# Optimization experiments

Measured on AMD Instinct MI355X. Metric: run time of the kernel, lower is better.

## Reference

```python
import jax, jax.numpy as jnp
import numpy as np

B, T, H, V = 512, 256, 512, 7  # batch, decode steps, hidden_size, output_size (LSTM input fixed at 7)


def setup_inputs() -> dict:
    key = jax.random.key(0)
    ks = jax.random.split(key, 9)
    s = 1.0 / np.sqrt(H)  # pytorch LSTM/Linear default uniform init scale
    tgt_ids = jax.random.randint(ks[0], (B, T), 0, V)
    target_onehot = jax.nn.one_hot(tgt_ids, V, dtype=jnp.float32)
    return {
        "h0": jax.random.normal(ks[1], (B, H), jnp.float32),
        "c0": jax.random.normal(ks[2], (B, H), jnp.float32),
        "target_onehot": target_onehot,
        "W_ih": jax.random.uniform(ks[3], (4 * H, V), jnp.float32, -s, s),
        "W_hh": jax.random.uniform(ks[4], (4 * H, H), jnp.float32, -s, s),
        "b_ih": jax.random.uniform(ks[5], (4 * H,), jnp.float32, -s, s),
        "b_hh": jax.random.uniform(ks[6], (4 * H,), jnp.float32, -s, s),
        "W_out": jax.random.uniform(ks[7], (V, H), jnp.float32, -s, s),
        "b_out": jax.random.uniform(ks[8], (V,), jnp.float32, -s, s),
    }


def reference(h0, c0, target_onehot, W_ih, W_hh, b_ih, b_hh, W_out, b_out):
    # Faithful to DecoderRNN.forward with target_onehot given:
    #  - torch.rand(1)<0 is always False => teacher forcing never used
    #  - topi==5 early break only applies when target_onehot is None
    # => deterministic greedy decode: x0 = target_onehot[:,0], x_{t+1} = one_hot(argmax(logits_t))
    T_ = target_onehot.shape[1]
    bias = b_ih + b_hh

    def step(carry, _):
        h, c, x = carry  # h,c: [B,H]; x: [B,V]
        xr = jax.nn.relu(x)  # F.relu(input) in forward_step
        gates = xr @ W_ih.T + h @ W_hh.T + bias  # [B,4H], torch gate order i,f,g,o
        i_, f_, g_, o_ = jnp.split(gates, 4, axis=-1)
        c_new = jax.nn.sigmoid(f_) * c + jax.nn.sigmoid(i_) * jnp.tanh(g_)
        h_new = jax.nn.sigmoid(o_) * jnp.tanh(c_new)
        out = h_new @ W_out.T + b_out  # [B,V]
        nxt = jax.nn.one_hot(jnp.argmax(out, axis=-1), out.shape[-1], dtype=out.dtype)
        return (h_new, c_new, nxt), out

    (hT, cT, _), outs = jax.lax.scan(step, (h0, c0, target_onehot[:, 0]), None, length=T_)
    logp = jax.nn.log_softmax(jnp.transpose(outs, (1, 0, 2)), axis=-1)  # [B,T,V]
    return logp, hT, cT
```

## Files before the change

### kernel.cpp

```cpp
#include <hip/hip_runtime.h>
#include <hip/hip_bf16.h>
#include <math.h>

#define Bn 512
#define Tn 256
#define Hn 512
#define Vn 7
#define BH (Bn*Hn)
#define NLP (Bn*Tn*Vn)

#define NBLK 256
#define NTHR 512
#define NGRP 16
#define GBLK 16
#define CNT_STRIDE 32

#define RST 132
#define REDH (32*RST)


typedef short short8 __attribute__((ext_vector_type(8)));
typedef float f32x4  __attribute__((ext_vector_type(4)));

__device__ __forceinline__ float sigf(float x){ return 1.0f/(1.0f + expf(-x)); }

__device__ __forceinline__ void bsplit(float x, short &h, short &m, short &l){
    __hip_bfloat16 bh = __float2bfloat16(x);
    float fh = __bfloat162float(bh);
    float r1 = x - fh;
    __hip_bfloat16 bm = __float2bfloat16(r1);
    float fm = __bfloat162float(bm);
    float r2 = r1 - fm;
    __hip_bfloat16 bl = __float2bfloat16(r2);
    h = __builtin_bit_cast(short, bh);
    m = __builtin_bit_cast(short, bm);
    l = __builtin_bit_cast(short, bl);
}

struct Trip { short8 h, m, l; };

__device__ __forceinline__ Trip split8(const float4 &a, const float4 &b){
    Trip t;
    const float v[8] = {a.x, a.y, a.z, a.w, b.x, b.y, b.z, b.w};
    #pragma unroll
    for (int e = 0; e < 8; ++e){
        short hh, mm, ll;
        bsplit(v[e], hh, mm, ll);
        t.h[e] = hh; t.m[e] = mm; t.l[e] = ll;
    }
    return t;
}

__device__ __forceinline__ void group_barrier(int* cnt, int target){
    __syncthreads();
    if (threadIdx.x == 0){
        __hip_atomic_fetch_add(cnt, 1, __ATOMIC_RELEASE, __HIP_MEMORY_SCOPE_AGENT);
        while (__hip_atomic_load(cnt, __ATOMIC_RELAXED, __HIP_MEMORY_SCOPE_AGENT) < target)
            __builtin_amdgcn_s_sleep(1);
        (void)__hip_atomic_load(cnt, __ATOMIC_ACQUIRE, __HIP_MEMORY_SCOPE_AGENT);
    }
    __syncthreads();
}

__global__ void init_kernel(float* lp, int* cnts){
    int i = blockIdx.x*blockDim.x + threadIdx.x;
    if (i < NGRP) cnts[i*CNT_STRIDE] = 0;
    for (int x = i; x < NLP; x += (int)(gridDim.x*blockDim.x)) lp[x] = 0.0f;
}

__global__ void __launch_bounds__(NTHR, 2)
decoder_rnn_kernel(const float* __restrict__ h0, const float* __restrict__ c0,
                   const float* __restrict__ tgt, const float* __restrict__ Wih,
                   const float* __restrict__ Whh, const float* __restrict__ bih,
                   const float* __restrict__ bhh, const float* __restrict__ Wout,
                   const float* __restrict__ bout, float* out, float* ws)
{
    __shared__ float red[2*32*RST];
    __shared__ float hn_lds[32*33];
    __shared__ int   idx_lds[32];

    float* hbuf = ws;
    float* cws  = ws + 2*BH;
    int*   cnts = (int*)(ws + 3*BH);
    float* lp   = out;

    const int idx = blockIdx.x;
    const int jt  = ((idx & 7) << 1) | ((idx >> 7) & 1);
    const int bt  = (idx >> 3) & 15;
    const int b0  = bt << 5;
    const int j0  = jt << 5;

    const int tid  = threadIdx.x;
    const int wv   = tid >> 6;
    const int lane = tid & 63;
    const int kh   = wv & 1;
    const int gp   = wv >> 1;
    const int lr   = lane & 15;
    const int lk   = lane >> 4;
    int* cnt = cnts + bt*CNT_STRIDE;

    const int lg_bl = tid / 7, lg_v = tid % 7;

    long aoff0, aoff1, woff0, woff1;
    {
        const int kb = (kh << 8) + (lk << 3);
        aoff0 = (long)(b0 + lr)*Hn + kb;
        aoff1 = aoff0 + (long)16*Hn;
        woff0 = (long)((gp << 9) + j0 + lr)*Hn + kb;
        woff1 = woff0 + (long)16*Hn;
    }

    #pragma unroll
    for (int i = 0; i < 8; ++i){
        const int f = tid + (i << 9);
        const int r = f >> 7, c4 = f & 127;
        *(float4*)(hbuf + (long)(b0 + r)*Hn + (c4 << 2)) =
            *(const float4*)(h0 + (long)(b0 + r)*Hn + (c4 << 2));
    }
    if (tid < 256){
        const int r = tid >> 3, c4 = tid & 7;
        *(float4*)(cws + (long)(b0 + r)*Hn + j0 + (c4 << 2)) =
            *(const float4*)(c0 + (long)(b0 + r)*Hn + j0 + (c4 << 2));
    }
    __syncthreads();

    for (int t = 0; t < Tn; ++t){
        const float* hprev = hbuf + (t & 1)*BH;
        float*       hnext = hbuf + ((t + 1) & 1)*BH;

        if (tid < 32){
            const int  bl = tid;
            const long b  = b0 + bl;
            float best; int am = 0;
            if (t == 0){
                const float* xp = tgt + (b*Tn)*Vn;
                best = xp[0];
                #pragma unroll
                for (int v = 1; v < Vn; ++v){ float xv = xp[v]; if (xv > best){ best = xv; am = v; } }
            } else {
                const float* xp = lp + (b*Tn + (t-1))*Vn;
                best = xp[0] + bout[0];
                #pragma unroll
                for (int v = 1; v < Vn; ++v){ float xv = xp[v] + bout[v]; if (xv > best){ best = xv; am = v; } }
            }
            idx_lds[bl] = am;
        }

        f32x4 acc00 = {0.f,0.f,0.f,0.f}, acc01 = {0.f,0.f,0.f,0.f};
        f32x4 acc10 = {0.f,0.f,0.f,0.f}, acc11 = {0.f,0.f,0.f,0.f};
        float4 rA[4][2][2], rB[4][2][2];

        #pragma unroll
        for (int p = 0; p < 2; ++p){
            const int ko = p << 5;
            rA[p][0][0] = *(const float4*)(hprev + aoff0 + ko);
            rA[p][0][1] = *(const float4*)(hprev + aoff0 + ko + 4);
            rA[p][1][0] = *(const float4*)(hprev + aoff1 + ko);
            rA[p][1][1] = *(const float4*)(hprev + aoff1 + ko + 4);
            rB[p][0][0] = *(const float4*)(Whh + woff0 + ko);
            rB[p][0][1] = *(const float4*)(Whh + woff0 + ko + 4);
            rB[p][1][0] = *(const float4*)(Whh + woff1 + ko);
            rB[p][1][1] = *(const float4*)(Whh + woff1 + ko + 4);
        }

        #pragma unroll 4
        for (int ks = 0; ks < 8; ++ks){
            const int cb = ks & 3;
            if (ks < 6){
                const int nb2 = (ks + 2) & 3;
                const int ko  = (ks + 2) << 5;
                rA[nb2][0][0] = *(const float4*)(hprev + aoff0 + ko);
                rA[nb2][0][1] = *(const float4*)(hprev + aoff0 + ko + 4);
                rA[nb2][1][0] = *(const float4*)(hprev + aoff1 + ko);
                rA[nb2][1][1] = *(const float4*)(hprev + aoff1 + ko + 4);
                rB[nb2][0][0] = *(const float4*)(Whh + woff0 + ko);
                rB[nb2][0][1] = *(const float4*)(Whh + woff0 + ko + 4);
                rB[nb2][1][0] = *(const float4*)(Whh + woff1 + ko);
                rB[nb2][1][1] = *(const float4*)(Whh + woff1 + ko + 4);
            }

            const Trip A0 = split8(rA[cb][0][0], rA[cb][0][1]);
            const Trip A1 = split8(rA[cb][1][0], rA[cb][1][1]);
            const Trip W0 = split8(rB[cb][0][0], rB[cb][0][1]);
            const Trip W1 = split8(rB[cb][1][0], rB[cb][1][1]);

            #define MM(ap, wp) \
                acc00 = __builtin_amdgcn_mfma_f32_16x16x32_bf16(A0.ap, W0.wp, acc00, 0,0,0); \
                acc01 = __builtin_amdgcn_mfma_f32_16x16x32_bf16(A0.ap, W1.wp, acc01, 0,0,0); \
                acc10 = __builtin_amdgcn_mfma_f32_16x16x32_bf16(A1.ap, W0.wp, acc10, 0,0,0); \
                acc11 = __builtin_amdgcn_mfma_f32_16x16x32_bf16(A1.ap, W1.wp, acc11, 0,0,0);
            MM(h,h) MM(h,m) MM(m,h) MM(h,l) MM(m,m) MM(l,h)
            #undef MM
        }

        {
            float* rp = red + kh*REDH + (gp << 5) + lr;
            const int bb = lk << 2;
            #pragma unroll
            for (int r = 0; r < 4; ++r){
                rp[(bb + r)*RST]           = acc00[r];
                rp[(bb + r)*RST + 16]      = acc01[r];
                rp[(16 + bb + r)*RST]      = acc10[r];
                rp[(16 + bb + r)*RST + 16] = acc11[r];
            }
        }
        __syncthreads();

        {
            const int b  = tid >> 4;
            const int jp = tid & 15;
            const int ix = idx_lds[b];
            float ga[4], gb_[4];
            #pragma unroll
            for (int g = 0; g < 4; ++g){
                const float2 v0 = *(const float2*)&red[       b*RST + (g << 5) + (jp << 1)];
                const float2 v1 = *(const float2*)&red[REDH + b*RST + (g << 5) + (jp << 1)];
                ga[g]  = v0.x + v1.x;
                gb_[g] = v0.y + v1.y;
            }
            #pragma unroll
            for (int u = 0; u < 2; ++u){
                const int j = (jp << 1) + u;
                float g4[4];
                #pragma unroll
                for (int g = 0; g < 4; ++g){
                    const int r = (g << 9) + j0 + j;
                    const float s = u ? gb_[g] : ga[g];
                    g4[g] = s + (Wih[r*Vn + ix] + bih[r] + bhh[r]);
                }
                const long bg = b0 + b;
                const int  jj = j0 + j;
                const float iv = sigf(g4[0]);
                const float fv = sigf(g4[1]);
                const float gv = tanhf(g4[2]);
                const float ov = sigf(g4[3]);
                const float cold = cws[bg*Hn + jj];
                const float cn2 = fv*cold + iv*gv;
                cws[bg*Hn + jj] = cn2;
                const float hn = ov * tanhf(cn2);
                hnext[bg*Hn + jj] = hn;
                hn_lds[b*33 + j] = hn;
            }
        }
        __syncthreads();

        if (tid < 224){
            const float* wo = Wout + lg_v*Hn + j0;
            float s = 0.0f;
            #pragma unroll
            for (int jj = 0; jj < 32; ++jj)
                s = fmaf(hn_lds[lg_bl*33 + jj], wo[jj], s);
            atomicAdd(&lp[((long)(b0 + lg_bl)*Tn + t)*Vn + lg_v], s);
        }

        group_barrier(cnt, GBLK*(t+1));
    }

    {
        const int r0 = b0 + (jt << 1);
        #pragma unroll
        for (int rr = 0; rr < 2; ++rr){
            const long hb = (long)(r0 + rr)*Hn;
            out[NLP + hb + tid]      = hbuf[hb + tid];
            out[NLP + BH + hb + tid] = cws[hb + tid];
        }
        const long row = (long)(r0 + (tid >> 8))*Tn + (tid & 255);
        float x[Vn]; float m = -INFINITY;
        #pragma unroll
        for (int v = 0; v < Vn; ++v){ x[v] = lp[row*Vn + v] + bout[v]; m = fmaxf(m, x[v]); }
        float s = 0.0f;
        #pragma unroll
        for (int v = 0; v < Vn; ++v) s += expf(x[v] - m);
        const float ls = logf(s);
        #pragma unroll
        for (int v = 0; v < Vn; ++v) lp[row*Vn + v] = x[v] - m - ls;
    }
}

extern "C" void kernel_launch(void* const* d_in, const int* in_sizes, int n_in,
                              void* d_out, int out_size, void* d_ws, size_t ws_size,
                              hipStream_t stream) {
    const float* h0   = (const float*)d_in[0];
    const float* c0   = (const float*)d_in[1];
    const float* tgt  = (const float*)d_in[2];
    const float* Wih  = (const float*)d_in[3];
    const float* Whh  = (const float*)d_in[4];
    const float* bih  = (const float*)d_in[5];
    const float* bhh  = (const float*)d_in[6];
    const float* Wout = (const float*)d_in[7];
    const float* bout = (const float*)d_in[8];
    float* out = (float*)d_out;
    float* ws  = (float*)d_ws;
    int*   cnts = (int*)(ws + 3*BH);

    init_kernel<<<256, 256, 0, stream>>>(out, cnts);

    decoder_rnn_kernel<<<dim3(NBLK), dim3(NTHR), 0, stream>>>(
        h0, c0, tgt, Wih, Whh, bih, bhh, Wout, bout, out, ws);
}
```

Before: 5.580 ms.

## Pre-split W_hh and hidden state into bf16 triplets stored in workspace

Adds a pre-kernel that splits W_hh once into hi/mid/lo bf16 planes, and has the recurrent kernel write the new hidden state as three bf16 planes each step. The MFMA loop then loads short8 planes directly instead of loading fp32 and splitting every step. This removes the per-step conversion ALU work for both operands, but raises load bytes by 1.5x (three 2-byte planes instead of one 4-byte value) and adds extra stores of the split hidden state. The new path is used only when the workspace is large enough, otherwise the old path runs.

```diff
diff --git a/kernel.cpp b/kernel.cpp
--- a/kernel.cpp
+++ b/kernel.cpp
@@ -8,6 +8,7 @@
 #define Vn 7
 #define BH (Bn*Hn)
 #define NLP (Bn*Tn*Vn)
+#define WSZ (4*Hn*Hn)
 
 #define NBLK 256
 #define NTHR 512
@@ -68,6 +69,17 @@
     for (int x = i; x < NLP; x += (int)(gridDim.x*blockDim.x)) lp[x] = 0.0f;
 }
 
+__global__ void wsplit_kernel(const float* __restrict__ Whh, float* ws){
+    short* hs  = (short*)(ws + 3*BH + 1024);
+    short* wsp = hs + 2*3*BH;
+    int i = blockIdx.x*blockDim.x + threadIdx.x;
+    for (int x = i; x < WSZ; x += (int)(gridDim.x*blockDim.x)){
+        short h, m, l; bsplit(Whh[x], h, m, l);
+        wsp[x] = h; wsp[WSZ + x] = m; wsp[2*WSZ + x] = l;
+    }
+}
+
+template<bool PS>
 __global__ void __launch_bounds__(NTHR, 2)
 decoder_rnn_kernel(const float* __restrict__ h0, const float* __restrict__ c0,
                    const float* __restrict__ tgt, const float* __restrict__ Wih,
@@ -82,6 +94,8 @@
     float* hbuf = ws;
     float* cws  = ws + 2*BH;
     int*   cnts = (int*)(ws + 3*BH);
+    short* hs   = (short*)(ws + 3*BH + 1024);
+    short* wsp  = hs + 2*3*BH;
     float* lp   = out;
 
     const int idx = blockIdx.x;
@@ -121,6 +135,13 @@
         const int r = tid >> 3, c4 = tid & 7;
         *(float4*)(cws + (long)(b0 + r)*Hn + j0 + (c4 << 2)) =
             *(const float4*)(c0 + (long)(b0 + r)*Hn + j0 + (c4 << 2));
+    }
+    if (PS){
+        for (int e = tid; e < 32*Hn; e += NTHR){
+            const long gi = (long)(b0 + (e >> 9))*Hn + (e & 511);
+            short h, m, l; bsplit(h0[gi], h, m, l);
+            hs[gi] = h; hs[BH + gi] = m; hs[2*BH + gi] = l;
+        }
     }
     __syncthreads();
 
@@ -148,49 +169,88 @@
 
         f32x4 acc00 = {0.f,0.f,0.f,0.f}, acc01 = {0.f,0.f,0.f,0.f};
         f32x4 acc10 = {0.f,0.f,0.f,0.f}, acc11 = {0.f,0.f,0.f,0.f};
-        float4 rA[4][2][2], rB[4][2][2];
-
-        #pragma unroll
-        for (int p = 0; p < 2; ++p){
-            const int ko = p << 5;
-            rA[p][0][0] = *(const float4*)(hprev + aoff0 + ko);
-            rA[p][0][1] = *(const float4*)(hprev + aoff0 + ko + 4);
-            rA[p][1][0] = *(const float4*)(hprev + aoff1 + ko);
-            rA[p][1][1] = *(const float4*)(hprev + aoff1 + ko + 4);
-            rB[p][0][0] = *(const float4*)(Whh + woff0 + ko);
-            rB[p][0][1] = *(const float4*)(Whh + woff0 + ko + 4);
-            rB[p][1][0] = *(const float4*)(Whh + woff1 + ko);
-            rB[p][1][1] = *(const float4*)(Whh + woff1 + ko + 4);
-        }
-
-        #pragma unroll 4
-        for (int ks = 0; ks < 8; ++ks){
-            const int cb = ks & 3;
-            if (ks < 6){
-                const int nb2 = (ks + 2) & 3;
-                const int ko  = (ks + 2) << 5;
-                rA[nb2][0][0] = *(const float4*)(hprev + aoff0 + ko);
-                rA[nb2][0][1] = *(const float4*)(hprev + aoff0 + ko + 4);
-                rA[nb2][1][0] = *(const float4*)(hprev + aoff1 + ko);
-                rA[nb2][1][1] = *(const float4*)(hprev + aoff1 + ko + 4);
-                rB[nb2][0][0] = *(const float4*)(Whh + woff0 + ko);
-                rB[nb2][0][1] = *(const float4*)(Whh + woff0 + ko + 4);
-                rB[nb2][1][0] = *(const float4*)(Whh + woff1 + ko);
-                rB[nb2][1][1] = *(const float4*)(Whh + woff1 + ko + 4);
-            }
-
-            const Trip A0 = split8(rA[cb][0][0], rA[cb][0][1]);
-            const Trip A1 = split8(rA[cb][1][0], rA[cb][1][1]);
-            const Trip W0 = split8(rB[cb][0][0], rB[cb][0][1]);
-            const Trip W1 = split8(rB[cb][1][0], rB[cb][1][1]);
-
-            #define MM(ap, wp) \
-                acc00 = __builtin_amdgcn_mfma_f32_16x16x32_bf16(A0.ap, W0.wp, acc00, 0,0,0); \
-                acc01 = __builtin_amdgcn_mfma_f32_16x16x32_bf16(A0.ap, W1.wp, acc01, 0,0,0); \
-                acc10 = __builtin_amdgcn_mfma_f32_16x16x32_bf16(A1.ap, W0.wp, acc10, 0,0,0); \
-                acc11 = __builtin_amdgcn_mfma_f32_16x16x32_bf16(A1.ap, W1.wp, acc11, 0,0,0);
-            MM(h,h) MM(h,m) MM(m,h) MM(h,l) MM(m,m) MM(l,h)
-            #undef MM
+
+        if (PS){
+            const short* AH = hs + (long)((t & 1)*3    )*BH;
+            const short* AM = hs + (long)((t & 1)*3 + 1)*BH;
+            const short* AL = hs + (long)((t & 1)*3 + 2)*BH;
+            short8 rA0[4][3], rA1[4][3], rW0[4][3], rW1[4][3];
+
+            #define LDSLOT(p, ko) \
+                rA0[p][0] = *(const short8*)(AH + aoff0 + (ko)); \
+                rA0[p][1] = *(const short8*)(AM + aoff0 + (ko)); \
+                rA0[p][2] = *(const short8*)(AL + aoff0 + (ko)); \
+                rA1[p][0] = *(const short8*)(AH + aoff1 + (ko)); \
+                rA1[p][1] = *(const short8*)(AM + aoff1 + (ko)); \
+                rA1[p][2] = *(const short8*)(AL + aoff1 + (ko)); \
+                rW0[p][0] = *(const short8*)(wsp +         woff0 + (ko)); \
+                rW0[p][1] = *(const short8*)(wsp + WSZ   + woff0 + (ko)); \
+                rW0[p][2] = *(const short8*)(wsp + 2*WSZ + woff0 + (ko)); \
+                rW1[p][0] = *(const short8*)(wsp +         woff1 + (ko)); \
+                rW1[p][1] = *(const short8*)(wsp + WSZ   + woff1 + (ko)); \
+                rW1[p][2] = *(const short8*)(wsp + 2*WSZ + woff1 + (ko));
+
+            LDSLOT(0, 0)
+            LDSLOT(1, 32)
+
+            #pragma unroll 4
+            for (int ks = 0; ks < 8; ++ks){
+                const int cb = ks & 3;
+                if (ks < 6){
+                    const int nb2 = (ks + 2) & 3;
+                    const int ko  = (ks + 2) << 5;
+                    LDSLOT(nb2, ko)
+                }
+                #define MM(ai, wi) \
+                    acc00 = __builtin_amdgcn_mfma_f32_16x16x32_bf16(rA0[cb][ai], rW0[cb][wi], acc00, 0,0,0); \
+                    acc01 = __builtin_amdgcn_mfma_f32_16x16x32_bf16(rA0[cb][ai], rW1[cb][wi], acc01, 0,0,0); \
+                    acc10 = __builtin_amdgcn_mfma_f32_16x16x32_bf16(rA1[cb][ai], rW0[cb][wi], acc10, 0,0,0); \
+                    acc11 = __builtin_amdgcn_mfma_f32_16x16x32_bf16(rA1[cb][ai], rW1[cb][wi], acc11, 0,0,0);
+                MM(0,0) MM(0,1) MM(1,0) MM(0,2) MM(1,1) MM(2,0)
+                #undef MM
+            }
+            #undef LDSLOT
+        } else {
+            float4 rA[4][2][2], rB[4][2][2];
+            #pragma unroll
+            for (int p = 0; p < 2; ++p){
+                const int ko = p << 5;
+                rA[p][0][0] = *(const float4*)(hprev + aoff0 + ko);
+                rA[p][0][1] = *(const float4*)(hprev + aoff0 + ko + 4);
+                rA[p][1][0] = *(const float4*)(hprev + aoff1 + ko);
+                rA[p][1][1] = *(const float4*)(hprev + aoff1 + ko + 4);
+                rB[p][0][0] = *(const float4*)(Whh + woff0 + ko);
+                rB[p][0][1] = *(const float4*)(Whh + woff0 + ko + 4);
+                rB[p][1][0] = *(const float4*)(Whh + woff1 + ko);
+                rB[p][1][1] = *(const float4*)(Whh + woff1 + ko + 4);
+            }
+            #pragma unroll 4
+            for (int ks = 0; ks < 8; ++ks){
+                const int cb = ks & 3;
+                if (ks < 6){
+                    const int nb2 = (ks + 2) & 3;
+                    const int ko  = (ks + 2) << 5;
+                    rA[nb2][0][0] = *(const float4*)(hprev + aoff0 + ko);
+                    rA[nb2][0][1] = *(const float4*)(hprev + aoff0 + ko + 4);
+                    rA[nb2][1][0] = *(const float4*)(hprev + aoff1 + ko);
+                    rA[nb2][1][1] = *(const float4*)(hprev + aoff1 + ko + 4);
+                    rB[nb2][0][0] = *(const float4*)(Whh + woff0 + ko);
+                    rB[nb2][0][1] = *(const float4*)(Whh + woff0 + ko + 4);
+                    rB[nb2][1][0] = *(const float4*)(Whh + woff1 + ko);
+                    rB[nb2][1][1] = *(const float4*)(Whh + woff1 + ko + 4);
+                }
+                const Trip A0 = split8(rA[cb][0][0], rA[cb][0][1]);
+                const Trip A1 = split8(rA[cb][1][0], rA[cb][1][1]);
+                const Trip W0 = split8(rB[cb][0][0], rB[cb][0][1]);
+                const Trip W1 = split8(rB[cb][1][0], rB[cb][1][1]);
+                #define MM(ap, wp) \
+                    acc00 = __builtin_amdgcn_mfma_f32_16x16x32_bf16(A0.ap, W0.wp, acc00, 0,0,0); \
+                    acc01 = __builtin_amdgcn_mfma_f32_16x16x32_bf16(A0.ap, W1.wp, acc01, 0,0,0); \
+                    acc10 = __builtin_amdgcn_mfma_f32_16x16x32_bf16(A1.ap, W0.wp, acc10, 0,0,0); \
+                    acc11 = __builtin_amdgcn_mfma_f32_16x16x32_bf16(A1.ap, W1.wp, acc11, 0,0,0);
+                MM(h,h) MM(h,m) MM(m,h) MM(h,l) MM(m,m) MM(l,h)
+                #undef MM
+            }
         }
 
         {
@@ -210,6 +270,7 @@
             const int b  = tid >> 4;
             const int jp = tid & 15;
             const int ix = idx_lds[b];
+            short* hsn = hs + (long)(((t + 1) & 1)*3)*BH;
             float ga[4], gb_[4];
             #pragma unroll
             for (int g = 0; g < 4; ++g){
@@ -240,6 +301,12 @@
                 const float hn = ov * tanhf(cn2);
                 hnext[bg*Hn + jj] = hn;
                 hn_lds[b*33 + j] = hn;
+                if (PS){
+                    short sh, sm2, sl; bsplit(hn, sh, sm2, sl);
+                    hsn[bg*Hn + jj]        = sh;
+                    hsn[BH + bg*Hn + jj]   = sm2;
+                    hsn[2*BH + bg*Hn + jj] = sl;
+                }
             }
         }
         __syncthreads();
@@ -295,6 +362,13 @@
 
     init_kernel<<<256, 256, 0, stream>>>(out, cnts);
 
-    decoder_rnn_kernel<<<dim3(NBLK), dim3(NTHR), 0, stream>>>(
-        h0, c0, tgt, Wih, Whh, bih, bhh, Wout, bout, out, ws);
-}
+    const size_t need = (size_t)(3*BH + 1024)*4 + (size_t)2*3*BH*2 + (size_t)3*WSZ*2;
+    if (ws_size >= need){
+        wsplit_kernel<<<1024, 256, 0, stream>>>(Whh, ws);
+        decoder_rnn_kernel<true><<<dim3(NBLK), dim3(NTHR), 0, stream>>>(
+            h0, c0, tgt, Wih, Whh, bih, bhh, Wout, bout, out, ws);
+    } else {
+        decoder_rnn_kernel<false><<<dim3(NBLK), dim3(NTHR), 0, stream>>>(
+            h0, c0, tgt, Wih, Whh, bih, bhh, Wout, bout, out, ws);
+    }
+}
```

Result: slower. 8.354 ms (+49.7%).
